# Optimization experiments

Hardware: AMD Instinct MI355X
Metric: run time of the kernel (lower is better)

The kernel has to match this reference:

```python
import jax, jax.numpy as jnp
import numpy as np

N_BASIS = 20
R_MAX = 3.5

# e3nn normalize2mom constant for silu: 1/sqrt(E[silu(z)^2]), z~N(0,1) (analytic quadrature)
_trapz = getattr(np, "trapezoid", np.trapz)
_z = np.linspace(-12.0, 12.0, 100001)
_phi = np.exp(-0.5 * _z**2) / np.sqrt(2.0 * np.pi)
_silu = _z / (1.0 + np.exp(-_z))
SILU_CST = float(1.0 / np.sqrt(_trapz(_silu**2 * _phi, _z)))  # ~1.679


def norm_silu(x):
    return SILU_CST * jax.nn.silu(x)


def spherical_harmonics_lmax3(pos):
    # component-normalized real spherical harmonics up to l=3, e3nn axis convention (y up)
    u = pos / jnp.linalg.norm(pos, axis=-1, keepdims=True)
    x, y, z = u[..., 0], u[..., 1], u[..., 2]
    x2, y2, z2 = x * x, y * y, z * z
    s3, s5, s15 = jnp.sqrt(3.0), jnp.sqrt(5.0), jnp.sqrt(15.0)
    s7, s105 = jnp.sqrt(7.0), jnp.sqrt(105.0)
    s35_8, s21_8 = jnp.sqrt(35.0 / 8.0), jnp.sqrt(21.0 / 8.0)
    sh = [
        jnp.ones_like(x),                                                   # l=0
        s3 * x, s3 * y, s3 * z,                                             # l=1
        s15 * x * z, s15 * x * y, s5 * (y2 - 0.5 * (x2 + z2)),
        s15 * y * z, 0.5 * s15 * (z2 - x2),                                 # l=2
        s35_8 * x * (3.0 * z2 - x2), s105 * x * y * z,
        s21_8 * x * (5.0 * y2 - 1.0), 0.5 * s7 * y * (5.0 * y2 - 3.0),
        s21_8 * z * (5.0 * y2 - 1.0), 0.5 * s105 * y * (z2 - x2),
        s35_8 * z * (z2 - 3.0 * x2),                                        # l=3
    ]
    return jnp.stack(sh, axis=-1)  # [E, 16]


def soft_one_hot_gaussian(d):
    # e3nn soft_one_hot_linspace(start=0, end=3.5, number=20, basis='gaussian', cutoff=True)
    values = jnp.linspace(0.0, R_MAX, N_BASIS + 2)[1:-1]
    step = R_MAX / (N_BASIS + 1)
    diff = (d[:, None] - values[None, :]) / step
    return jnp.exp(-diff * diff) / 1.12


def setup_inputs() -> dict:
    E, N = 2_000_000, 125_000
    key = jax.random.key(0)
    k = jax.random.split(key, 6)
    return {
        "pos": jax.random.normal(k[0], (E, 3), jnp.float32),
        "x_right": jax.random.normal(k[1], (E, 1), jnp.float32),
        "x_left": jax.random.normal(k[2], (N, 1), jnp.float32),
        "W1": jax.random.normal(k[3], (20, 30), jnp.float32),
        "W2": jax.random.normal(k[4], (30, 5), jnp.float32),
        "origin_index": jax.random.randint(k[5], (E,), 0, N),
    }


def reference(pos, x_right, x_left, W1, W2, origin_index):
    sh = spherical_harmonics_lmax3(pos)                 # [E, 16], component norm
    d = jnp.linalg.norm(pos, axis=-1)                   # [E]
    emb = soft_one_hot_gaussian(d)                      # [E, 20]
    # e3nn FullyConnectedNet([20, 30, 5], silu): x @ W / sqrt(fan_in), normalized act on hidden
    h = norm_silu(emb @ (W1 / jnp.sqrt(jnp.asarray(W1.shape[0], jnp.float32))))
    tp_weights = h @ (W2 / jnp.sqrt(jnp.asarray(W2.shape[0], jnp.float32)))  # [E, 5]
    # tp1: FullyConnectedTensorProduct('1x0e', sh, '5x0e'): only CG path is 0e(x)0e->0e
    # (single path -> path-normalization factor 1; Y_0 = 1 under component normalization)
    h_right = tp_weights * x_right * sh[:, :1]          # [E, 5]
    # tp2: FullTensorProduct('1x0e', '5x0e') -> '5x0e': plain scalar product per channel
    product = x_left[origin_index] * h_right            # [E, 5]
    return jnp.sum(product)
```

## Files before the change

kernel.cpp:

```cpp
#include <hip/hip_runtime.h>


#define TN   2048
#define DMAXF 5.0f
#define NBLK 4096
#define TPB  256

__device__ __constant__ float kSiluCst = 1.6765581f;

__global__ __launch_bounds__(256) void build_lut_kernel(
    const float* __restrict__ W1, const float* __restrict__ W2,
    float* __restrict__ table)
{
    int t = blockIdx.x * 256 + threadIdx.x;
    int entry = t >> 5;
    int k = t & 31;
    int kk = (k < 30) ? k : 29;

    float d  = (float)entry * (DMAXF / (float)TN);
    float t6 = 6.0f * d;
    const float w1scale = 1.0f / (1.12f * sqrtf(20.0f));

    float a = 0.0f;
    #pragma unroll
    for (int j = 0; j < 20; ++j) {
        float df = t6 - (float)(j + 1);
        float e  = __expf(-df * df);
        a = fmaf(e * w1scale, W1[j * 30 + kk], a);
    }
    float s = a / (1.0f + __expf(-a));

    float w2s = 0.0f;
    #pragma unroll
    for (int c = 0; c < 5; ++c) w2s += W2[kk * 5 + c];

    float contrib = (k < 30) ? s * w2s * (kSiluCst / sqrtf(30.0f)) : 0.0f;

    #pragma unroll
    for (int m = 16; m > 0; m >>= 1) contrib += __shfl_xor(contrib, m, 32);

    if (k == 0 && entry < TN) table[entry] = contrib;
}

__global__ __launch_bounds__(TPB) void edge_sum_kernel(
    const float* __restrict__ pos, const float* __restrict__ xr,
    const float* __restrict__ xl, const int* __restrict__ oi,
    const float* __restrict__ table, double* __restrict__ partials, int E)
{
    __shared__ float lut[TN];
    __shared__ double swv[TPB / 64];

    {
        const float4* t4 = (const float4*)table;
        float4* l4 = (float4*)lut;
        l4[threadIdx.x]       = t4[threadIdx.x];
        l4[threadIdx.x + TPB] = t4[threadIdx.x + TPB];
    }
    __syncthreads();

    const float scale = (float)TN / DMAXF;
    const float umax  = (float)(TN - 1) - 1e-3f;

    double acc = 0.0;
    int stride = gridDim.x * TPB;
    for (int e = blockIdx.x * TPB + threadIdx.x; e < E; e += stride) {
        float x = pos[3 * e + 0];
        float y = pos[3 * e + 1];
        float z = pos[3 * e + 2];
        float d  = sqrtf(fmaf(x, x, fmaf(y, y, z * z)));
        float u  = fminf(d * scale, umax);
        int   i0 = (int)u;
        float fr = u - (float)i0;
        float f0 = lut[i0];
        float f1 = lut[i0 + 1];
        float f  = fmaf(fr, f1 - f0, f0);
        acc += (double)(f * xr[e] * xl[oi[e]]);
    }

    #pragma unroll
    for (int off = 32; off > 0; off >>= 1) acc += __shfl_down(acc, off);
    int lane = threadIdx.x & 63, wv = threadIdx.x >> 6;
    if (lane == 0) swv[wv] = acc;
    __syncthreads();
    if (threadIdx.x == 0)
        partials[blockIdx.x] = (swv[0] + swv[1]) + (swv[2] + swv[3]);
}

__global__ __launch_bounds__(256) void final_reduce_kernel(
    const double* __restrict__ partials, int n, float* __restrict__ out)
{
    __shared__ double sm[256];
    double a = 0.0;
    for (int i = threadIdx.x; i < n; i += 256) a += partials[i];
    sm[threadIdx.x] = a;
    __syncthreads();
    #pragma unroll
    for (int s = 128; s > 0; s >>= 1) {
        if (threadIdx.x < (unsigned)s) sm[threadIdx.x] += sm[threadIdx.x + s];
        __syncthreads();
    }
    if (threadIdx.x == 0) out[0] = (float)sm[0];
}

extern "C" void kernel_launch(void* const* d_in, const int* in_sizes, int n_in,
                              void* d_out, int out_size, void* d_ws, size_t ws_size,
                              hipStream_t stream) {
    const float* pos = (const float*)d_in[0];
    const float* xr  = (const float*)d_in[1];
    const float* xl  = (const float*)d_in[2];
    const float* W1  = (const float*)d_in[3];
    const float* W2  = (const float*)d_in[4];
    const int*   oi  = (const int*)d_in[5];
    float* out = (float*)d_out;

    int E = in_sizes[1];

    float*  table    = (float*)d_ws;
    double* partials = (double*)((char*)d_ws + (size_t)TN * sizeof(float));

    hipLaunchKernelGGL(build_lut_kernel, dim3((TN * 32) / 256), dim3(256), 0, stream,
                       W1, W2, table);
    hipLaunchKernelGGL(edge_sum_kernel, dim3(NBLK), dim3(TPB), 0, stream,
                       pos, xr, xl, oi, table, partials, E);
    hipLaunchKernelGGL(final_reduce_kernel, dim3(1), dim3(256), 0, stream,
                       partials, NBLK, out);
}
```

Measured before the change: 28.78 us.

## Stage pos tiles in LDS with float4 loads, process four edges per thread

The edge kernel now gives each block one 1024-edge tile. The block stages that tile's pos data into shared memory with coalesced float4 loads, and each thread handles four consecutive edges using vectorized xr and origin_index loads. The grid grows from a fixed 4096 blocks to about E/1024, so the final reduce must sum about 1954 partials instead of 4096. Each thread accumulates in float and converts to double only per thread, and the extra shared memory could lower occupancy.

```diff
diff --git a/kernel.cpp b/kernel.cpp
--- a/kernel.cpp
+++ b/kernel.cpp
@@ -1,10 +1,10 @@
 #include <hip/hip_runtime.h>
 
 
-#define TN   2048
+#define TN    2048
 #define DMAXF 5.0f
-#define NBLK 4096
-#define TPB  256
+#define TPB   256
+#define TILE  1024
 
 __device__ __constant__ float kSiluCst = 1.6765581f;
 
@@ -48,41 +48,90 @@
     const float* __restrict__ table, double* __restrict__ partials, int E)
 {
     __shared__ float lut[TN];
+    __shared__ float lpos[3 * TILE];
     __shared__ double swv[TPB / 64];
+
+    const int tid = threadIdx.x;
+    const long tile0 = (long)blockIdx.x * TILE;
 
     {
         const float4* t4 = (const float4*)table;
         float4* l4 = (float4*)lut;
-        l4[threadIdx.x]       = t4[threadIdx.x];
-        l4[threadIdx.x + TPB] = t4[threadIdx.x + TPB];
+        l4[tid]       = t4[tid];
+        l4[tid + TPB] = t4[tid + TPB];
+    }
+    {
+        const long  gbase4 = (tile0 * 3) / 4;
+        const long  lim4   = (3L * E) / 4;
+        const float4* g4 = (const float4*)pos;
+        float4* l4 = (float4*)lpos;
+        #pragma unroll
+        for (int i = 0; i < 3; ++i) {
+            int li = tid + i * TPB;
+            long gi = gbase4 + li;
+            if (gi < lim4) l4[li] = g4[gi];
+        }
+        long tail = lim4 * 4 + tid;
+        if (tail < 3L * E && tail >= tile0 * 3 && tail < tile0 * 3 + 3 * TILE)
+            lpos[tail - tile0 * 3] = pos[tail];
     }
     __syncthreads();
 
     const float scale = (float)TN / DMAXF;
     const float umax  = (float)(TN - 1) - 1e-3f;
 
+    const int rem = (int)min((long)TILE, (long)E - tile0);
+    const int e0  = tid * 4;
     double acc = 0.0;
-    int stride = gridDim.x * TPB;
-    for (int e = blockIdx.x * TPB + threadIdx.x; e < E; e += stride) {
-        float x = pos[3 * e + 0];
-        float y = pos[3 * e + 1];
-        float z = pos[3 * e + 2];
-        float d  = sqrtf(fmaf(x, x, fmaf(y, y, z * z)));
-        float u  = fminf(d * scale, umax);
-        int   i0 = (int)u;
-        float fr = u - (float)i0;
-        float f0 = lut[i0];
-        float f1 = lut[i0 + 1];
-        float f  = fmaf(fr, f1 - f0, f0);
-        acc += (double)(f * xr[e] * xl[oi[e]]);
+
+    if (e0 + 4 <= rem) {
+        const float4* lp4 = (const float4*)lpos;
+        float4 a = lp4[3 * tid + 0];
+        float4 b = lp4[3 * tid + 1];
+        float4 c = lp4[3 * tid + 2];
+        float4 xv = ((const float4*)(xr + tile0))[tid];
+        int4   ov = ((const int4*)(oi + tile0))[tid];
+
+        float px[4] = {a.x, a.w, b.z, c.y};
+        float py[4] = {a.y, b.x, b.w, c.z};
+        float pz[4] = {a.z, b.y, c.x, c.w};
+        float xrv[4] = {xv.x, xv.y, xv.z, xv.w};
+        float xlv[4];
+        xlv[0] = xl[ov.x]; xlv[1] = xl[ov.y]; xlv[2] = xl[ov.z]; xlv[3] = xl[ov.w];
+
+        float fsum = 0.0f;
+        #pragma unroll
+        for (int j = 0; j < 4; ++j) {
+            float d  = sqrtf(fmaf(px[j], px[j], fmaf(py[j], py[j], pz[j] * pz[j])));
+            float u  = fminf(d * scale, umax);
+            int   i0 = (int)u;
+            float fr = u - (float)i0;
+            float f  = fmaf(fr, lut[i0 + 1] - lut[i0], lut[i0]);
+            fsum = fmaf(f * xrv[j], xlv[j], fsum);
+        }
+        acc = (double)fsum;
+    } else if (e0 < rem) {
+        float fsum = 0.0f;
+        for (int j = 0; j < 4 && e0 + j < rem; ++j) {
+            int le = e0 + j;
+            float x = lpos[3 * le], y = lpos[3 * le + 1], z = lpos[3 * le + 2];
+            float d  = sqrtf(fmaf(x, x, fmaf(y, y, z * z)));
+            float u  = fminf(d * scale, umax);
+            int   i0 = (int)u;
+            float fr = u - (float)i0;
+            float f  = fmaf(fr, lut[i0 + 1] - lut[i0], lut[i0]);
+            long  ge = tile0 + le;
+            fsum = fmaf(f * xr[ge], xl[oi[ge]], fsum);
+        }
+        acc = (double)fsum;
     }
 
     #pragma unroll
     for (int off = 32; off > 0; off >>= 1) acc += __shfl_down(acc, off);
-    int lane = threadIdx.x & 63, wv = threadIdx.x >> 6;
+    int lane = tid & 63, wv = tid >> 6;
     if (lane == 0) swv[wv] = acc;
     __syncthreads();
-    if (threadIdx.x == 0)
+    if (tid == 0)
         partials[blockIdx.x] = (swv[0] + swv[1]) + (swv[2] + swv[3]);
 }
 
@@ -114,14 +163,15 @@
     float* out = (float*)d_out;
 
     int E = in_sizes[1];
+    int nblk = (E + TILE - 1) / TILE;
 
     float*  table    = (float*)d_ws;
     double* partials = (double*)((char*)d_ws + (size_t)TN * sizeof(float));
 
     hipLaunchKernelGGL(build_lut_kernel, dim3((TN * 32) / 256), dim3(256), 0, stream,
                        W1, W2, table);
-    hipLaunchKernelGGL(edge_sum_kernel, dim3(NBLK), dim3(TPB), 0, stream,
+    hipLaunchKernelGGL(edge_sum_kernel, dim3(nblk), dim3(TPB), 0, stream,
                        pos, xr, xl, oi, table, partials, E);
     hipLaunchKernelGGL(final_reduce_kernel, dim3(1), dim3(256), 0, stream,
-                       partials, NBLK, out);
+                       partials, nblk, out);
 }
```

Result: no change. 28.86 us (+0.3%).

## Fuse LUT build, edge sum and final reduce into one kernel with cubic LUT

Applied to the files above, without the earlier changes.

Replaces the three-kernel pipeline with a single kernel. Each block rebuilds a small 132-entry Catmull-Rom lookup table in shared memory from W1/W2, then processes a 1024-edge tile using vectorized float4 loads, and adds its result to the output with a float atomicAdd after a memset. The goal is to remove two kernel launches and the partials round trip, and to load edges more efficiently. The cost is redundant table computation in every one of roughly 1954 blocks (30x20 MACs per entry), plus a float atomic reduction that is nondeterministic and less precise than the old double reduction.

```diff
diff --git a/kernel.cpp b/kernel.cpp
--- a/kernel.cpp
+++ b/kernel.cpp
@@ -1,105 +1,129 @@
 #include <hip/hip_runtime.h>
 
 
-#define TN   2048
-#define DMAXF 5.0f
-#define NBLK 4096
-#define TPB  256
+#define TPB   256
+#define TILE  1024
+#define TNL   128
+#define TNLP  132
 
 __device__ __constant__ float kSiluCst = 1.6765581f;
 
-__global__ __launch_bounds__(256) void build_lut_kernel(
-    const float* __restrict__ W1, const float* __restrict__ W2,
-    float* __restrict__ table)
-{
-    int t = blockIdx.x * 256 + threadIdx.x;
-    int entry = t >> 5;
-    int k = t & 31;
-    int kk = (k < 30) ? k : 29;
-
-    float d  = (float)entry * (DMAXF / (float)TN);
-    float t6 = 6.0f * d;
-    const float w1scale = 1.0f / (1.12f * sqrtf(20.0f));
-
-    float a = 0.0f;
-    #pragma unroll
-    for (int j = 0; j < 20; ++j) {
-        float df = t6 - (float)(j + 1);
-        float e  = __expf(-df * df);
-        a = fmaf(e * w1scale, W1[j * 30 + kk], a);
-    }
-    float s = a / (1.0f + __expf(-a));
-
-    float w2s = 0.0f;
-    #pragma unroll
-    for (int c = 0; c < 5; ++c) w2s += W2[kk * 5 + c];
-
-    float contrib = (k < 30) ? s * w2s * (kSiluCst / sqrtf(30.0f)) : 0.0f;
-
-    #pragma unroll
-    for (int m = 16; m > 0; m >>= 1) contrib += __shfl_xor(contrib, m, 32);
-
-    if (k == 0 && entry < TN) table[entry] = contrib;
-}
-
-__global__ __launch_bounds__(TPB) void edge_sum_kernel(
+__global__ __launch_bounds__(TPB) void fused_edge_kernel(
     const float* __restrict__ pos, const float* __restrict__ xr,
     const float* __restrict__ xl, const int* __restrict__ oi,
-    const float* __restrict__ table, double* __restrict__ partials, int E)
+    const float* __restrict__ W1, const float* __restrict__ W2,
+    float* __restrict__ out, int E)
 {
-    __shared__ float lut[TN];
+    __shared__ float sW1[600];
+    __shared__ float sW2[150];
+    __shared__ float lut[TNLP];
     __shared__ double swv[TPB / 64];
 
-    {
-        const float4* t4 = (const float4*)table;
-        float4* l4 = (float4*)lut;
-        l4[threadIdx.x]       = t4[threadIdx.x];
-        l4[threadIdx.x + TPB] = t4[threadIdx.x + TPB];
+    const int  tid   = threadIdx.x;
+    const long tile0 = (long)blockIdx.x * TILE;
+    const int  rem   = (int)min((long)TILE, (long)E - tile0);
+    const int  e0    = tid * 4;
+    const bool full  = (e0 + 4 <= rem);
+
+    float4 pa, pb, pc, xv; int4 ov;
+    if (full) {
+        const float4* p4 = (const float4*)(pos + tile0 * 3);
+        pa = p4[3 * tid + 0];
+        pb = p4[3 * tid + 1];
+        pc = p4[3 * tid + 2];
+        xv = ((const float4*)(xr + tile0))[tid];
+        ov = ((const int4*)(oi + tile0))[tid];
+    }
+
+    if (tid < 200) {
+        sW1[tid]       = W1[tid];
+        sW1[tid + 200] = W1[tid + 200];
+        sW1[tid + 400] = W1[tid + 400];
+    }
+    if (tid < 150) sW2[tid] = W2[tid];
+    __syncthreads();
+
+    if (tid < TNLP) {
+        const float h   = 5.0f / (float)TNL;
+        const float d   = ((float)tid - 1.0f) * h;
+        const float t6  = 6.0f * d;
+        const float w1s = 1.0f / (1.12f * sqrtf(20.0f));
+        float emb[20];
+        #pragma unroll
+        for (int j = 0; j < 20; ++j) {
+            float df = t6 - (float)(j + 1);
+            emb[j] = __expf(-df * df) * w1s;
+        }
+        float facc = 0.0f;
+        for (int k = 0; k < 30; ++k) {
+            float a = 0.0f;
+            #pragma unroll
+            for (int j = 0; j < 20; ++j) a = fmaf(emb[j], sW1[j * 30 + k], a);
+            float s   = a / (1.0f + __expf(-a));
+            float w2s = sW2[k*5+0] + sW2[k*5+1] + sW2[k*5+2] + sW2[k*5+3] + sW2[k*5+4];
+            facc = fmaf(s, w2s, facc);
+        }
+        lut[tid] = facc * (kSiluCst / sqrtf(30.0f));
     }
     __syncthreads();
 
-    const float scale = (float)TN / DMAXF;
-    const float umax  = (float)(TN - 1) - 1e-3f;
+    const float invh = (float)TNL / 5.0f;
+    const float umax = (float)(TNL + 1) + 0.999f;
+    double acc = 0.0;
 
-    double acc = 0.0;
-    int stride = gridDim.x * TPB;
-    for (int e = blockIdx.x * TPB + threadIdx.x; e < E; e += stride) {
-        float x = pos[3 * e + 0];
-        float y = pos[3 * e + 1];
-        float z = pos[3 * e + 2];
-        float d  = sqrtf(fmaf(x, x, fmaf(y, y, z * z)));
-        float u  = fminf(d * scale, umax);
-        int   i0 = (int)u;
-        float fr = u - (float)i0;
-        float f0 = lut[i0];
-        float f1 = lut[i0 + 1];
-        float f  = fmaf(fr, f1 - f0, f0);
-        acc += (double)(f * xr[e] * xl[oi[e]]);
+    if (full) {
+        float px[4] = {pa.x, pa.w, pb.z, pc.y};
+        float py[4] = {pa.y, pb.x, pb.w, pc.z};
+        float pz[4] = {pa.z, pb.y, pc.x, pc.w};
+        float xrv[4] = {xv.x, xv.y, xv.z, xv.w};
+        float xlv[4];
+        xlv[0] = xl[ov.x]; xlv[1] = xl[ov.y]; xlv[2] = xl[ov.z]; xlv[3] = xl[ov.w];
+
+        float fsum = 0.0f;
+        #pragma unroll
+        for (int j = 0; j < 4; ++j) {
+            float d = sqrtf(fmaf(px[j], px[j], fmaf(py[j], py[j], pz[j] * pz[j])));
+            float u = fminf(fmaf(d, invh, 1.0f), umax);
+            int   i0 = (int)u;
+            float t  = u - (float)i0;
+            float p0 = lut[i0 - 1], p1 = lut[i0], p2 = lut[i0 + 1], p3 = lut[i0 + 2];
+            float w0 = 0.5f * t * ((2.0f - t) * t - 1.0f);
+            float w1 = 0.5f * (t * t * (3.0f * t - 5.0f) + 2.0f);
+            float w2 = 0.5f * t * ((4.0f - 3.0f * t) * t + 1.0f);
+            float w3 = 0.5f * t * t * (t - 1.0f);
+            float f  = w0 * p0 + w1 * p1 + w2 * p2 + w3 * p3;
+            fsum = fmaf(f * xrv[j], xlv[j], fsum);
+        }
+        acc = (double)fsum;
+    } else if (e0 < rem) {
+        float fsum = 0.0f;
+        for (int j = 0; j < 4 && e0 + j < rem; ++j) {
+            long  ge = tile0 + e0 + j;
+            float x = pos[3 * ge], y = pos[3 * ge + 1], z = pos[3 * ge + 2];
+            float d = sqrtf(fmaf(x, x, fmaf(y, y, z * z)));
+            float u = fminf(fmaf(d, invh, 1.0f), umax);
+            int   i0 = (int)u;
+            float t  = u - (float)i0;
+            float p0 = lut[i0 - 1], p1 = lut[i0], p2 = lut[i0 + 1], p3 = lut[i0 + 2];
+            float w0 = 0.5f * t * ((2.0f - t) * t - 1.0f);
+            float w1 = 0.5f * (t * t * (3.0f * t - 5.0f) + 2.0f);
+            float w2 = 0.5f * t * ((4.0f - 3.0f * t) * t + 1.0f);
+            float w3 = 0.5f * t * t * (t - 1.0f);
+            float f  = w0 * p0 + w1 * p1 + w2 * p2 + w3 * p3;
+            fsum = fmaf(f * xr[ge], xl[oi[ge]], fsum);
+        }
+        acc = (double)fsum;
     }
 
     #pragma unroll
     for (int off = 32; off > 0; off >>= 1) acc += __shfl_down(acc, off);
-    int lane = threadIdx.x & 63, wv = threadIdx.x >> 6;
+    int lane = tid & 63, wv = tid >> 6;
     if (lane == 0) swv[wv] = acc;
     __syncthreads();
-    if (threadIdx.x == 0)
-        partials[blockIdx.x] = (swv[0] + swv[1]) + (swv[2] + swv[3]);
-}
-
-__global__ __launch_bounds__(256) void final_reduce_kernel(
-    const double* __restrict__ partials, int n, float* __restrict__ out)
-{
-    __shared__ double sm[256];
-    double a = 0.0;
-    for (int i = threadIdx.x; i < n; i += 256) a += partials[i];
-    sm[threadIdx.x] = a;
-    __syncthreads();
-    #pragma unroll
-    for (int s = 128; s > 0; s >>= 1) {
-        if (threadIdx.x < (unsigned)s) sm[threadIdx.x] += sm[threadIdx.x + s];
-        __syncthreads();
+    if (tid == 0) {
+        double bsum = (swv[0] + swv[1]) + (swv[2] + swv[3]);
+        atomicAdd(out, (float)bsum);
     }
-    if (threadIdx.x == 0) out[0] = (float)sm[0];
 }
 
 extern "C" void kernel_launch(void* const* d_in, const int* in_sizes, int n_in,
@@ -114,14 +138,9 @@
     float* out = (float*)d_out;
 
     int E = in_sizes[1];
+    int nblk = (E + TILE - 1) / TILE;
 
-    float*  table    = (float*)d_ws;
-    double* partials = (double*)((char*)d_ws + (size_t)TN * sizeof(float));
-
-    hipLaunchKernelGGL(build_lut_kernel, dim3((TN * 32) / 256), dim3(256), 0, stream,
-                       W1, W2, table);
-    hipLaunchKernelGGL(edge_sum_kernel, dim3(NBLK), dim3(TPB), 0, stream,
-                       pos, xr, xl, oi, table, partials, E);
-    hipLaunchKernelGGL(final_reduce_kernel, dim3(1), dim3(256), 0, stream,
-                       partials, NBLK, out);
+    hipMemsetAsync(out, 0, sizeof(float), stream);
+    hipLaunchKernelGGL(fused_edge_kernel, dim3(nblk), dim3(TPB), 0, stream,
+                       pos, xr, xl, oi, W1, W2, out, E);
 }
```

Measured after the change: 50.38 us. 1.75x slower.
